# Kernel optimization log

Measured on AMD Instinct MI355X. Metric: run time of the kernel, lower is better.

## Reference

```python
import jax, jax.numpy as jnp
import numpy as np

N = 65536        # tokens (x.size(0) loop in original)
EMBED = 2048     # embed_dim
FFN = 8          # ffn_dim == n_qubits (required by out[i] = measure(qdev) broadcast)


def setup_inputs() -> dict:
    key = jax.random.key(0)
    k1, k2, k3, k4, k5 = jax.random.split(key, 5)
    s1 = 1.0 / np.sqrt(EMBED)
    s2 = 1.0 / np.sqrt(FFN)
    return {
        "x": jax.random.normal(k1, (N, EMBED), dtype=jnp.float32),
        "W1": jax.random.uniform(k2, (FFN, EMBED), jnp.float32, -s1, s1),
        "b1": jax.random.uniform(k3, (FFN,), jnp.float32, -s1, s1),
        "W2": jax.random.uniform(k4, (EMBED, FFN), jnp.float32, -s2, s2),
        "b2": jax.random.uniform(k5, (EMBED,), jnp.float32, -s2, s2),
    }


def reference(x, W1, b1, W2, b2):
    # h = relu(linear1(x)); dropout is identity at eval time.
    h = jax.nn.relu(jnp.einsum("ne,fe->nf", x, W1) + b1)          # [N, FFN]
    # Quantum circuit per token: on each wire w, Rx(h[w]) then Ry(h[w % FFN] == h[w])
    # applied to |0>, followed by <PauliZ>. Product state => analytic expval:
    # <Z> = cos(rx_angle) * cos(ry_angle) = cos(h)^2.
    c = jnp.cos(h)
    q = c * c                                                      # [N, FFN]
    return jnp.einsum("nf,ef->ne", q, W2) + b2                      # [N, EMBED]
```

## Files before the change

### kernel.cpp

```cpp
#include <hip/hip_runtime.h>


static constexpr int EMBED = 2048;
static constexpr int FFN   = 8;
static constexpr int TPB   = 64;
static constexpr int CH    = 32;
static constexpr int NCH   = EMBED / CH;
static constexpr int RS    = 36;

__global__ __launch_bounds__(256, 4)
void qffn_kernel(const float* __restrict__ x, const float* __restrict__ W1,
                 const float* __restrict__ b1, const float* __restrict__ W2,
                 const float* __restrict__ b2, float* __restrict__ out)
{
    __shared__ float smem[4 * TPB * RS + TPB * 12];
    float* xt = smem;
    float* qb = smem + 4 * TPB * RS;

    const int tid  = threadIdx.x;
    const int lane = tid & 63;
    const int wv   = __builtin_amdgcn_readfirstlane(tid >> 6);
    const int n0   = blockIdx.x * TPB;

    const int id1  = tid + 256;
    const int row0 = tid >> 3, col0 = (tid & 7) << 2;
    const int row1 = id1 >> 3, col1 = (id1 & 7) << 2;
    const float* xp0 = x + (long)(n0 + row0) * EMBED + col0;
    const float* xp1 = x + (long)(n0 + row1) * EMBED + col1;

    float4 r0 = *(const float4*)(xp0);
    float4 r1 = *(const float4*)(xp1);

    const int f0 = 2 * wv, f1 = f0 + 1;
    const float* w1a = W1 + f0 * EMBED;
    const float* w1b = W1 + f1 * EMBED;

    float h0 = 0.f, h1 = 0.f;

    for (int c = 0; c < NCH; ++c) {
        __syncthreads();
        *(float4*)(xt + row0 * RS + col0) = r0;
        *(float4*)(xt + row1 * RS + col1) = r1;
        if (c + 1 < NCH) {
            r0 = *(const float4*)(xp0 + (c + 1) * CH);
            r1 = *(const float4*)(xp1 + (c + 1) * CH);
        }
        __syncthreads();

        float xv[CH];
        #pragma unroll
        for (int j = 0; j < CH / 4; ++j) {
            float4 v = *(const float4*)(xt + lane * RS + 4 * j);
            xv[4*j+0] = v.x; xv[4*j+1] = v.y; xv[4*j+2] = v.z; xv[4*j+3] = v.w;
        }
        const int e0 = c * CH;
        #pragma unroll
        for (int j = 0; j < CH; ++j) {
            h0 = fmaf(xv[j], w1a[e0 + j], h0);
            h1 = fmaf(xv[j], w1b[e0 + j], h1);
        }
    }

    h0 = fmaxf(h0 + b1[f0], 0.f);
    h1 = fmaxf(h1 + b1[f1], 0.f);
    float c0 = __cosf(h0), c1 = __cosf(h1);

    qb[lane * 12 + f0] = c0 * c0;
    qb[lane * 12 + f1] = c1 * c1;
    __syncthreads();
    float q[FFN];
    #pragma unroll
    for (int f = 0; f < FFN; ++f) q[f] = qb[lane * 12 + f];

    float* ot = smem + wv * (TPB * RS);
    for (int cc = 0; cc < NCH / 4; ++cc) {
        const int e0 = (cc * 4 + wv) * CH;
        float o[CH];
        #pragma unroll
        for (int j = 0; j < CH; ++j) {
            float acc = b2[e0 + j];
            #pragma unroll
            for (int f = 0; f < FFN; ++f)
                acc = fmaf(q[f], W2[(e0 + j) * FFN + f], acc);
            o[j] = acc;
        }
        #pragma unroll
        for (int j = 0; j < CH / 4; ++j)
            *(float4*)(ot + lane * RS + 4 * j) =
                make_float4(o[4*j], o[4*j+1], o[4*j+2], o[4*j+3]);
        __syncthreads();
        #pragma unroll
        for (int k = 0; k < 8; ++k) {
            const int id  = k * 64 + lane;
            const int row = id >> 3, c4 = (id & 7) << 2;
            float4 v = *(const float4*)(ot + row * RS + c4);
            *(float4*)(out + (long)(n0 + row) * EMBED + e0 + c4) = v;
        }
        __syncthreads();
    }
}

extern "C" void kernel_launch(void* const* d_in, const int* in_sizes, int n_in,
                              void* d_out, int out_size, void* d_ws, size_t ws_size,
                              hipStream_t stream) {
    const float* x  = (const float*)d_in[0];
    const float* W1 = (const float*)d_in[1];
    const float* b1 = (const float*)d_in[2];
    const float* W2 = (const float*)d_in[3];
    const float* b2 = (const float*)d_in[4];
    float* out = (float*)d_out;

    const int ntok = in_sizes[0] / EMBED;
    qffn_kernel<<<dim3(ntok / TPB), dim3(256), 0, stream>>>(x, W1, b1, W2, b2, out);
}
```

Before: 1.028 ms.

## Replace LDS-staged tiles with 8-lane-per-token direct loads and shuffle reduction

Drops the shared-memory transpose staging and all block barriers. Each token is now handled by 8 lanes that read x and W1 directly as float4, accumulate all 8 FFN dot products, and reduce them with xor shuffles. The second projection writes float4 outputs straight to global memory, and occupancy hints and tokens per block change as well. This removes LDS traffic and barrier stalls in a memory-bound kernel. The cost is more redundant W1 and W2 loads per lane, which have to be served from cache, and heavier register use with 32 accumulators.

Measured after the change: 1.450 ms. +41.1%, slower.

```diff
diff --git a/kernel.cpp b/kernel.cpp
--- a/kernel.cpp
+++ b/kernel.cpp
@@ -3,100 +3,72 @@
 
 static constexpr int EMBED = 2048;
 static constexpr int FFN   = 8;
-static constexpr int TPB   = 64;
-static constexpr int CH    = 32;
-static constexpr int NCH   = EMBED / CH;
-static constexpr int RS    = 36;
+static constexpr int TPB   = 32;
 
-__global__ __launch_bounds__(256, 4)
+__global__ __launch_bounds__(256, 6)
 void qffn_kernel(const float* __restrict__ x, const float* __restrict__ W1,
                  const float* __restrict__ b1, const float* __restrict__ W2,
                  const float* __restrict__ b2, float* __restrict__ out)
 {
-    __shared__ float smem[4 * TPB * RS + TPB * 12];
-    float* xt = smem;
-    float* qb = smem + 4 * TPB * RS;
+    const int tid = threadIdx.x;
+    const int sub = tid & 7;
+    const int t   = blockIdx.x * TPB + (tid >> 3);
+    const long rowbase = (long)t * EMBED;
 
-    const int tid  = threadIdx.x;
-    const int lane = tid & 63;
-    const int wv   = __builtin_amdgcn_readfirstlane(tid >> 6);
-    const int n0   = blockIdx.x * TPB;
+    const float* xp  = x + rowbase + sub * 4;
+    const float* w1p = W1 + sub * 4;
 
-    const int id1  = tid + 256;
-    const int row0 = tid >> 3, col0 = (tid & 7) << 2;
-    const int row1 = id1 >> 3, col1 = (id1 & 7) << 2;
-    const float* xp0 = x + (long)(n0 + row0) * EMBED + col0;
-    const float* xp1 = x + (long)(n0 + row1) * EMBED + col1;
+    float4 h[FFN];
+    #pragma unroll
+    for (int f = 0; f < FFN; ++f) h[f] = make_float4(0.f, 0.f, 0.f, 0.f);
 
-    float4 r0 = *(const float4*)(xp0);
-    float4 r1 = *(const float4*)(xp1);
-
-    const int f0 = 2 * wv, f1 = f0 + 1;
-    const float* w1a = W1 + f0 * EMBED;
-    const float* w1b = W1 + f1 * EMBED;
-
-    float h0 = 0.f, h1 = 0.f;
-
-    for (int c = 0; c < NCH; ++c) {
-        __syncthreads();
-        *(float4*)(xt + row0 * RS + col0) = r0;
-        *(float4*)(xt + row1 * RS + col1) = r1;
-        if (c + 1 < NCH) {
-            r0 = *(const float4*)(xp0 + (c + 1) * CH);
-            r1 = *(const float4*)(xp1 + (c + 1) * CH);
-        }
-        __syncthreads();
-
-        float xv[CH];
+    #pragma unroll 2
+    for (int c = 0; c < EMBED / 32; ++c) {
+        const float4 xv = *(const float4*)(xp + c * 32);
         #pragma unroll
-        for (int j = 0; j < CH / 4; ++j) {
-            float4 v = *(const float4*)(xt + lane * RS + 4 * j);
-            xv[4*j+0] = v.x; xv[4*j+1] = v.y; xv[4*j+2] = v.z; xv[4*j+3] = v.w;
-        }
-        const int e0 = c * CH;
-        #pragma unroll
-        for (int j = 0; j < CH; ++j) {
-            h0 = fmaf(xv[j], w1a[e0 + j], h0);
-            h1 = fmaf(xv[j], w1b[e0 + j], h1);
+        for (int f = 0; f < FFN; ++f) {
+            const float4 wv = *(const float4*)(w1p + f * EMBED + c * 32);
+            h[f].x = fmaf(xv.x, wv.x, h[f].x);
+            h[f].y = fmaf(xv.y, wv.y, h[f].y);
+            h[f].z = fmaf(xv.z, wv.z, h[f].z);
+            h[f].w = fmaf(xv.w, wv.w, h[f].w);
         }
     }
 
-    h0 = fmaxf(h0 + b1[f0], 0.f);
-    h1 = fmaxf(h1 + b1[f1], 0.f);
-    float c0 = __cosf(h0), c1 = __cosf(h1);
-
-    qb[lane * 12 + f0] = c0 * c0;
-    qb[lane * 12 + f1] = c1 * c1;
-    __syncthreads();
     float q[FFN];
     #pragma unroll
-    for (int f = 0; f < FFN; ++f) q[f] = qb[lane * 12 + f];
+    for (int f = 0; f < FFN; ++f) {
+        float s = (h[f].x + h[f].y) + (h[f].z + h[f].w);
+        s += __shfl_xor(s, 1);
+        s += __shfl_xor(s, 2);
+        s += __shfl_xor(s, 4);
+        s = fmaxf(s + b1[f], 0.f);
+        const float cv = __cosf(s);
+        q[f] = cv * cv;
+    }
 
-    float* ot = smem + wv * (TPB * RS);
-    for (int cc = 0; cc < NCH / 4; ++cc) {
-        const int e0 = (cc * 4 + wv) * CH;
-        float o[CH];
+    #pragma unroll 2
+    for (int c = 0; c < EMBED / 32; ++c) {
+        const int e = c * 32 + sub * 4;
+        const float4 bv = *(const float4*)(b2 + e);
+        const float bvs[4] = {bv.x, bv.y, bv.z, bv.w};
+        float o[4];
         #pragma unroll
-        for (int j = 0; j < CH; ++j) {
-            float acc = b2[e0 + j];
-            #pragma unroll
-            for (int f = 0; f < FFN; ++f)
-                acc = fmaf(q[f], W2[(e0 + j) * FFN + f], acc);
-            o[j] = acc;
+        for (int j = 0; j < 4; ++j) {
+            const float4 wlo = *(const float4*)(W2 + (e + j) * FFN);
+            const float4 whi = *(const float4*)(W2 + (e + j) * FFN + 4);
+            float s = bvs[j];
+            s = fmaf(q[0], wlo.x, s);
+            s = fmaf(q[1], wlo.y, s);
+            s = fmaf(q[2], wlo.z, s);
+            s = fmaf(q[3], wlo.w, s);
+            s = fmaf(q[4], whi.x, s);
+            s = fmaf(q[5], whi.y, s);
+            s = fmaf(q[6], whi.z, s);
+            s = fmaf(q[7], whi.w, s);
+            o[j] = s;
         }
-        #pragma unroll
-        for (int j = 0; j < CH / 4; ++j)
-            *(float4*)(ot + lane * RS + 4 * j) =
-                make_float4(o[4*j], o[4*j+1], o[4*j+2], o[4*j+3]);
-        __syncthreads();
-        #pragma unroll
-        for (int k = 0; k < 8; ++k) {
-            const int id  = k * 64 + lane;
-            const int row = id >> 3, c4 = (id & 7) << 2;
-            float4 v = *(const float4*)(ot + row * RS + c4);
-            *(float4*)(out + (long)(n0 + row) * EMBED + e0 + c4) = v;
-        }
-        __syncthreads();
+        *(float4*)(out + rowbase + e) = make_float4(o[0], o[1], o[2], o[3]);
     }
 }
 
```
